# Kernel tuning notes

Measured on AMD Instinct MI355X. Metric: run time of the kernel, lower is better.

## Reference

```python
import jax, jax.numpy as jnp
import numpy as np

H = 16  # num_heads (inner_dim 1024 // default head_dim 64)
D = 64  # head_dim
EPS = 1e-5

def layernorm(x, w, b):
    mu = jnp.mean(x, axis=-1, keepdims=True)
    var = jnp.var(x, axis=-1, keepdims=True)
    return (x - mu) * jax.lax.rsqrt(var + EPS) * w + b

def attention(x, kv, wq, wk, wv, wo, bo):
    b, t, c = x.shape
    s = kv.shape[1]
    q = (x @ wq).reshape(b, t, H, D).transpose(0, 2, 1, 3)   # bhtd
    k = (kv @ wk).reshape(b, s, H, D).transpose(0, 2, 1, 3)  # bhsd
    v = (kv @ wv).reshape(b, s, H, D).transpose(0, 2, 1, 3)
    scores = jnp.einsum('bhqd,bhkd->bhqk', q, k) * (D ** -0.5)
    attn = jax.nn.softmax(scores, axis=-1)
    out = jnp.einsum('bhqk,bhkd->bhqd', attn, v)
    out = out.transpose(0, 2, 1, 3).reshape(b, t, c)
    return out @ wo + bo

def setup_inputs() -> dict:
    key = jax.random.key(0)
    ks = jax.random.split(key, 16)
    hs = 1024
    dff = 4 * hs  # 4096
    sc = lambda fan_in: 1.0 / np.sqrt(fan_in)
    inp = {
        'x': jax.random.normal(ks[0], (2, 2048, hs), jnp.float32),
        'encoder_hidden_states': jax.random.normal(ks[1], (2, 512, 64), jnp.float32),
        'ln1_w': jnp.ones((hs,), jnp.float32), 'ln1_b': jnp.zeros((hs,), jnp.float32),
        'a1_wq': jax.random.normal(ks[2], (hs, hs), jnp.float32) * sc(hs),
        'a1_wk': jax.random.normal(ks[3], (hs, hs), jnp.float32) * sc(hs),
        'a1_wv': jax.random.normal(ks[4], (hs, hs), jnp.float32) * sc(hs),
        'a1_wo': jax.random.normal(ks[5], (hs, hs), jnp.float32) * sc(hs),
        'a1_bo': jnp.zeros((hs,), jnp.float32),
        'ln2_w': jnp.ones((hs,), jnp.float32), 'ln2_b': jnp.zeros((hs,), jnp.float32),
        'a2_wq': jax.random.normal(ks[6], (hs, hs), jnp.float32) * sc(hs),
        'a2_wk': jax.random.normal(ks[7], (64, hs), jnp.float32) * sc(64),
        'a2_wv': jax.random.normal(ks[8], (64, hs), jnp.float32) * sc(64),
        'a2_wo': jax.random.normal(ks[9], (hs, hs), jnp.float32) * sc(hs),
        'a2_bo': jnp.zeros((hs,), jnp.float32),
        'ln3_w': jnp.ones((hs,), jnp.float32), 'ln3_b': jnp.zeros((hs,), jnp.float32),
        'ff_w1': jax.random.normal(ks[10], (hs, 2 * dff), jnp.float32) * sc(hs),
        'ff_b1': jnp.zeros((2 * dff,), jnp.float32),
        'ff_w2': jax.random.normal(ks[11], (dff, hs), jnp.float32) * sc(dff),
        'ff_b2': jnp.zeros((hs,), jnp.float32),
    }
    return inp

def reference(x, encoder_hidden_states, ln1_w, ln1_b, a1_wq, a1_wk, a1_wv, a1_wo, a1_bo,
              ln2_w, ln2_b, a2_wq, a2_wk, a2_wv, a2_wo, a2_bo,
              ln3_w, ln3_b, ff_w1, ff_b1, ff_w2, ff_b2):
    # self-attention sub-block
    h = layernorm(x, ln1_w, ln1_b)
    x = x + attention(h, h, a1_wq, a1_wk, a1_wv, a1_wo, a1_bo)
    # cross-attention sub-block (kv from encoder_hidden_states, dim 64)
    h = layernorm(x, ln2_w, ln2_b)
    x = x + attention(h, encoder_hidden_states, a2_wq, a2_wk, a2_wv, a2_wo, a2_bo)
    # GEGLU feed-forward sub-block
    h = layernorm(x, ln3_w, ln3_b)
    hp = h @ ff_w1 + ff_b1
    h1, h2 = jnp.split(hp, 2, axis=-1)
    h = (h1 * jax.nn.gelu(h2, approximate=False)) @ ff_w2 + ff_b2
    return x + h
```

## Files before the change

kernel.cpp:

```cpp
#include <hip/hip_runtime.h>
#include <hip/hip_bf16.h>
#include <stdint.h>

typedef unsigned short u16;
typedef __bf16 bf16x8 __attribute__((ext_vector_type(8)));
typedef float f32x4 __attribute__((ext_vector_type(4)));
typedef u16 u16x8 __attribute__((ext_vector_type(8)));
typedef u16 u16x4 __attribute__((ext_vector_type(4)));

__device__ __forceinline__ u16 f2bf(float f) {
  union { float f; uint32_t u; } v; v.f = f;
  uint32_t r = v.u + 0x7fffu + ((v.u >> 16) & 1u);
  return (u16)(r >> 16);
}
__device__ __forceinline__ float bf2f(u16 u) {
  union { uint32_t u; float f; } v; v.u = ((uint32_t)u) << 16;
  return v.f;
}
__device__ __forceinline__ uint32_t cvtpk(float a, float b) {
  uint32_t r;
  asm("v_cvt_pk_bf16_f32 %0, %1, %2" : "=v"(r) : "v"(a), "v"(b));
  return r;
}

__device__ __forceinline__ void gld16(const u16* g, u16* l) {
  __builtin_amdgcn_global_load_lds(
      (const __attribute__((address_space(1))) uint32_t*)g,
      (__attribute__((address_space(3))) uint32_t*)l, 16, 0, 0);
}

struct WB {
  const float* src[6];
  u16* dst[6];
  float scale[6];
};
__global__ void wconv_b(WB wb, int K, int N) {
  const int z = blockIdx.z;
  const float* __restrict__ W = wb.src[z];
  u16* __restrict__ Wt = wb.dst[z];
  const float scale = wb.scale[z];
  __shared__ float tile[32][33];
  const int n0 = blockIdx.x * 32, k0 = blockIdx.y * 32;
  const int tx = threadIdx.x, ty = threadIdx.y;
#pragma unroll
  for (int i = 0; i < 4; ++i)
    tile[ty + 8 * i][tx] = W[(size_t)(k0 + ty + 8 * i) * N + n0 + tx];
  __syncthreads();
#pragma unroll
  for (int i = 0; i < 4; ++i)
    Wt[(size_t)(n0 + ty + 8 * i) * K + k0 + tx] = f2bf(scale * tile[tx][ty + 8 * i]);
}

__global__ void wconv_t(const float* __restrict__ W, u16* __restrict__ Wt, int K, int N) {
  __shared__ float tile[32][33];
  const int n0 = blockIdx.x * 32, k0 = blockIdx.y * 32;
  const int tx = threadIdx.x, ty = threadIdx.y;
#pragma unroll
  for (int i = 0; i < 4; ++i)
    tile[ty + 8 * i][tx] = W[(size_t)(k0 + ty + 8 * i) * N + n0 + tx];
  __syncthreads();
#pragma unroll
  for (int i = 0; i < 4; ++i)
    Wt[(size_t)(n0 + ty + 8 * i) * K + k0 + tx] = f2bf(tile[tx][ty + 8 * i]);
}

__global__ void wconv_g(const float* __restrict__ W, u16* __restrict__ Wt) {
  __shared__ float tile[32][33];
  const int n0 = blockIdx.x * 32, k0 = blockIdx.y * 32;
  const int tx = threadIdx.x, ty = threadIdx.y;
#pragma unroll
  for (int i = 0; i < 4; ++i)
    tile[ty + 8 * i][tx] = W[(size_t)(k0 + ty + 8 * i) * 8192 + n0 + tx];
  __syncthreads();
#pragma unroll
  for (int i = 0; i < 4; ++i) {
    const int n = n0 + ty + 8 * i;
    const int half = n >> 12, c = n & 4095;
    const int blk = c >> 7, cc = c & 127;
    const int wcol = cc >> 5, rem = cc & 31;
    const int sub = rem >> 4, idx = rem & 15;
    const int p = blk * 256 + wcol * 64 + (sub * 2 + half) * 16 + idx;
    Wt[(size_t)p * 1024 + k0 + tx] = f2bf(tile[tx][ty + 8 * i]);
  }
}

__global__ void cvt_bf(const float* __restrict__ in, u16* __restrict__ out, int n) {
  int i = blockIdx.x * 256 + threadIdx.x;
  if (i < n) out[i] = f2bf(in[i]);
}

__global__ __launch_bounds__(256)
void vtrans(const u16* __restrict__ V, int ldv, int hoff, u16* __restrict__ Vt, int S) {
  __shared__ u16 tile[64][72];
  const int t0 = blockIdx.x, bh = blockIdx.y;
  const int b = bh >> 4, hc = (bh & 15) * 64 + hoff;
  const int tid = threadIdx.x;
  const int r = tid >> 2, dq = (tid & 3) * 16;
  const int pos = ((r >> 5) << 5) | (((r >> 2) & 3) << 3) | (((r >> 4) & 1) << 2) | (r & 3);
  const size_t grow = ((size_t)b * S + t0 * 64 + r) * ldv + hc + dq;
  u16x8 v1 = *(const u16x8*)&V[grow];
  u16x8 v2 = *(const u16x8*)&V[grow + 8];
#pragma unroll
  for (int j = 0; j < 8; ++j) {
    tile[dq + j][pos] = v1[j];
    tile[dq + 8 + j][pos] = v2[j];
  }
  __syncthreads();
  const int d = tid >> 2, c = (tid & 3) * 16;
  u16x8 o1, o2;
#pragma unroll
  for (int j = 0; j < 8; ++j) { o1[j] = tile[d][c + j]; o2[j] = tile[d][c + 8 + j]; }
  *(u16x8*)&Vt[((size_t)bh * 64 + d) * S + t0 * 64 + c] = o1;
  *(u16x8*)&Vt[((size_t)bh * 64 + d) * S + t0 * 64 + c + 8] = o2;
}

__global__ __launch_bounds__(256)
void ln_fwd(const float* __restrict__ X, const float* __restrict__ wt,
            const float* __restrict__ bs, u16* __restrict__ Y) {
  const int row = blockIdx.x, t = threadIdx.x;
  const float4 v = *(const float4*)&X[(size_t)row * 1024 + t * 4];
  float s = v.x + v.y + v.z + v.w;
  float s2 = v.x * v.x + v.y * v.y + v.z * v.z + v.w * v.w;
#pragma unroll
  for (int off = 32; off > 0; off >>= 1) {
    s += __shfl_xor(s, off);
    s2 += __shfl_xor(s2, off);
  }
  __shared__ float rs[4], rs2[4];
  const int w = t >> 6;
  if ((t & 63) == 0) { rs[w] = s; rs2[w] = s2; }
  __syncthreads();
  s = rs[0] + rs[1] + rs[2] + rs[3];
  s2 = rs2[0] + rs2[1] + rs2[2] + rs2[3];
  const float mu = s * (1.0f / 1024.0f);
  const float var = s2 * (1.0f / 1024.0f) - mu * mu;
  const float rstd = rsqrtf(var + 1e-5f);
  const float4 wv = *(const float4*)&wt[t * 4];
  const float4 bv = *(const float4*)&bs[t * 4];
  u16x4 o;
  o[0] = f2bf((v.x - mu) * rstd * wv.x + bv.x);
  o[1] = f2bf((v.y - mu) * rstd * wv.y + bv.y);
  o[2] = f2bf((v.z - mu) * rstd * wv.z + bv.z);
  o[3] = f2bf((v.w - mu) * rstd * wv.w + bv.w);
  *(u16x4*)&Y[(size_t)row * 1024 + t * 4] = o;
}

template<int TN>
__global__ __launch_bounds__(256, 4)
void gemm_bf16(const u16* __restrict__ A, int lda, const u16* __restrict__ Bt,
               int M, int N, int K, const float* __restrict__ bias,
               const float* __restrict__ resid, float oscale,
               float* __restrict__ outF, u16* __restrict__ outB) {
  constexpr int WNV = (TN == 128) ? 2 : 1;
  constexpr int WMV = 4 / WNV;
  constexpr int WM = 128 / WMV;
  constexpr int WN = TN / WNV;
  constexpr int MI = WM / 16, NI = WN / 16;
  __shared__ __align__(16) u16 Al[128 * 64];
  __shared__ __align__(16) u16 Bl[TN * 64];
  const int tid = threadIdx.x;
  const int w = tid >> 6, l = tid & 63, lo = l & 15, g = l >> 4;
  const int gx = gridDim.x, nwg = gx * gridDim.y;
  const int lin = blockIdx.y * gx + blockIdx.x;
  const int q = nwg >> 3, r = nwg & 7;
  const int xcd = lin & 7, pos = lin >> 3;
  const int sid = (xcd < r ? xcd * (q + 1) : r * (q + 1) + (xcd - r) * q) + pos;
  const int bm = (sid % gx) * 128, bn = (sid / gx) * TN;
  const int wm = (w / WNV) * WM, wn = (w % WNV) * WN;
  const int swz = (lo & 7) << 3;
  f32x4 acc[MI][NI] = {};

  for (int k0 = 0; k0 < K; k0 += 64) {
#pragma unroll
    for (int p = 0; p < 4; ++p) {
      int idx = p * 256 + tid;
      int row = idx >> 3, c = idx & 7;
      gld16(A + (size_t)(bm + row) * lda + k0 + ((c ^ (row & 7)) << 3), &Al[idx * 8]);
    }
#pragma unroll
    for (int p = 0; p < TN / 32; ++p) {
      int idx = p * 256 + tid;
      int row = idx >> 3, c = idx & 7;
      gld16(Bt + (size_t)(bn + row) * K + k0 + ((c ^ (row & 7)) << 3), &Bl[idx * 8]);
    }
    asm volatile("s_waitcnt vmcnt(0)" ::: "memory");
    __syncthreads();
#pragma unroll
    for (int ks = 0; ks < 2; ++ks) {
      bf16x8 af[MI], bf[NI];
#pragma unroll
      for (int i = 0; i < MI; ++i)
        af[i] = *(const bf16x8*)&Al[(wm + i * 16 + lo) * 64 + ((ks * 32 + g * 8) ^ swz)];
#pragma unroll
      for (int i = 0; i < NI; ++i)
        bf[i] = *(const bf16x8*)&Bl[(wn + i * 16 + lo) * 64 + ((ks * 32 + g * 8) ^ swz)];
#pragma unroll
      for (int mi = 0; mi < MI; ++mi)
#pragma unroll
        for (int ni = 0; ni < NI; ++ni)
          acc[mi][ni] = __builtin_amdgcn_mfma_f32_16x16x32_bf16(af[mi], bf[ni], acc[mi][ni], 0, 0, 0);
    }
    __syncthreads();
  }

#pragma unroll
  for (int mi = 0; mi < MI; ++mi) {
#pragma unroll
    for (int ni = 0; ni < NI; ++ni) {
      const int col = bn + wn + ni * 16 + lo;
      const float bb = bias ? bias[col] : 0.0f;
      const int row0 = bm + wm + mi * 16 + g * 4;
#pragma unroll
      for (int rr = 0; rr < 4; ++rr) {
        const size_t off = (size_t)(row0 + rr) * N + col;
        float v = acc[mi][ni][rr] * oscale + bb;
        if (resid) v += resid[off];
        if (outF) outF[off] = v;
        else outB[off] = f2bf(v);
      }
    }
  }
}

#define ST2(p0, p1, dst) { gld16(p0, (dst) + tid * 8); gld16(p1, (dst) + 4096 + tid * 8); (p0) += 64; (p1) += 64; }

template<int MODE>
__global__ __launch_bounds__(512, 2)
void gemm256(const u16* __restrict__ A, int lda, const u16* __restrict__ Bt,
             int M, int N, int K, const float* __restrict__ bias,
             const float* __restrict__ resid, float oscale,
             float* __restrict__ outF, u16* __restrict__ outB) {
  __shared__ __align__(16) u16 sm[65536];
  const int tid = threadIdx.x;
  const int w = tid >> 6, l = tid & 63, lo = l & 15, g = l >> 4;
  const int wrow = w >> 2, wcol = w & 3;
  const int gx = gridDim.x;
  const int nwg = gx * gridDim.y;
  const int lin = blockIdx.y * gx + blockIdx.x;
  const int q = nwg >> 3, r = nwg & 7;
  const int xcd = lin & 7, pos = lin >> 3;
  const int sid = (xcd < r ? xcd * (q + 1) : r * (q + 1) + (xcd - r) * q) + pos;
  const int bm = (sid % gx) * 256, bn = (sid / gx) * 256;

  const int NT = K >> 6;
  const int swz = (lo & 7) << 3;
  f32x4 acc[8][4] = {};

  const int sr8 = tid >> 3;
  const int sc8 = ((tid & 7) ^ (sr8 & 7)) << 3;
  const u16 *pA0 = A + (size_t)(bm + sr8) * lda + sc8;
  const u16 *pA1 = A + (size_t)(bm + 64 + sr8) * lda + sc8;
  const u16 *pA2 = A + (size_t)(bm + 128 + sr8) * lda + sc8;
  const u16 *pA3 = A + (size_t)(bm + 192 + sr8) * lda + sc8;
  const u16 *pB0 = Bt + (size_t)(bn + sr8) * K + sc8;
  const u16 *pB1 = Bt + (size_t)(bn + 64 + sr8) * K + sc8;
  const u16 *pB2 = Bt + (size_t)(bn + 128 + sr8) * K + sc8;
  const u16 *pB3 = Bt + (size_t)(bn + 192 + sr8) * K + sc8;

  ST2(pB0, pB1, sm + 16384);
  ST2(pB2, pB3, sm + 16384 + 8192);
  ST2(pA0, pA1, sm);
  ST2(pA2, pA3, sm + 8192);
  if (NT > 1) {
    ST2(pB0, pB1, sm + 32768 + 16384);
    ST2(pB2, pB3, sm + 32768 + 16384 + 8192);
    ST2(pA0, pA1, sm + 32768);
  }
  asm volatile("s_waitcnt vmcnt(6)" ::: "memory");
  __builtin_amdgcn_s_barrier();

  for (int t = 0; t < NT; ++t) {
    u16* Ab_ = sm + (t & 1) * 32768;
    u16* Bb_ = Ab_ + 16384;
    bf16x8 a0[4][2], a1[4][2], bfr[4][2];
#pragma unroll
    for (int mf = 0; mf < 4; ++mf) {
      const int rowi = wrow * 128 + mf * 16 + lo;
#pragma unroll
      for (int kk = 0; kk < 2; ++kk)
        a0[mf][kk] = *(const bf16x8*)&Ab_[rowi * 64 + ((kk * 32 + g * 8) ^ swz)];
    }
#pragma unroll
    for (int nf = 0; nf < 4; ++nf) {
      const int rowi = wcol * 64 + nf * 16 + lo;
#pragma unroll
      for (int kk = 0; kk < 2; ++kk)
        bfr[nf][kk] = *(const bf16x8*)&Bb_[rowi * 64 + ((kk * 32 + g * 8) ^ swz)];
    }
    if (t + 1 < NT)
      ST2(pA2, pA3, sm + ((t + 1) & 1) * 32768 + 8192);
    __builtin_amdgcn_s_barrier();
    __builtin_amdgcn_s_setprio(1);
#pragma unroll
    for (int mf = 0; mf < 4; ++mf)
#pragma unroll
      for (int nf = 0; nf < 2; ++nf)
#pragma unroll
        for (int kk = 0; kk < 2; ++kk)
          acc[mf][nf] = __builtin_amdgcn_mfma_f32_16x16x32_bf16(a0[mf][kk], bfr[nf][kk], acc[mf][nf], 0, 0, 0);
    __builtin_amdgcn_s_setprio(0);
    __builtin_amdgcn_s_barrier();
#pragma unroll
    for (int mf = 0; mf < 4; ++mf) {
      const int rowi = wrow * 128 + 64 + mf * 16 + lo;
#pragma unroll
      for (int kk = 0; kk < 2; ++kk)
        a1[mf][kk] = *(const bf16x8*)&Ab_[rowi * 64 + ((kk * 32 + g * 8) ^ swz)];
    }
    if (t + 2 < NT)
      ST2(pB0, pB1, sm + (t & 1) * 32768 + 16384);
    __builtin_amdgcn_s_barrier();
    __builtin_amdgcn_s_setprio(1);
#pragma unroll
    for (int mf = 0; mf < 4; ++mf)
#pragma unroll
      for (int nf = 2; nf < 4; ++nf)
#pragma unroll
        for (int kk = 0; kk < 2; ++kk)
          acc[mf][nf] = __builtin_amdgcn_mfma_f32_16x16x32_bf16(a0[mf][kk], bfr[nf][kk], acc[mf][nf], 0, 0, 0);
    __builtin_amdgcn_s_setprio(0);
    __builtin_amdgcn_s_barrier();
    if (t + 2 < NT)
      ST2(pB2, pB3, sm + (t & 1) * 32768 + 16384 + 8192);
    __builtin_amdgcn_s_barrier();
    __builtin_amdgcn_s_setprio(1);
#pragma unroll
    for (int mf = 0; mf < 4; ++mf)
#pragma unroll
      for (int nf = 0; nf < 2; ++nf)
#pragma unroll
        for (int kk = 0; kk < 2; ++kk)
          acc[4 + mf][nf] = __builtin_amdgcn_mfma_f32_16x16x32_bf16(a1[mf][kk], bfr[nf][kk], acc[4 + mf][nf], 0, 0, 0);
    __builtin_amdgcn_s_setprio(0);
    __builtin_amdgcn_s_barrier();
    if (t + 2 < NT)
      ST2(pA0, pA1, sm + (t & 1) * 32768);
    __builtin_amdgcn_s_barrier();
    __builtin_amdgcn_s_setprio(1);
#pragma unroll
    for (int mf = 0; mf < 4; ++mf)
#pragma unroll
      for (int nf = 2; nf < 4; ++nf)
#pragma unroll
        for (int kk = 0; kk < 2; ++kk)
          acc[4 + mf][nf] = __builtin_amdgcn_mfma_f32_16x16x32_bf16(a1[mf][kk], bfr[nf][kk], acc[4 + mf][nf], 0, 0, 0);
    __builtin_amdgcn_s_setprio(0);
    if (t + 2 < NT) asm volatile("s_waitcnt vmcnt(6)" ::: "memory");
    else            asm volatile("s_waitcnt vmcnt(0)" ::: "memory");
    __builtin_amdgcn_s_barrier();
  }

  if (MODE == 1) {
    const int obase = bn >> 1;
#pragma unroll
    for (int mi = 0; mi < 8; ++mi) {
#pragma unroll
      for (int sub = 0; sub < 2; ++sub) {
        const int col = obase + wcol * 32 + sub * 16 + lo;
        const float b1 = bias[col];
        const float b2 = bias[4096 + col];
#pragma unroll
        for (int rr = 0; rr < 4; ++rr) {
          const int rowi = wrow * 128 + mi * 16 + g * 4 + rr;
          const float h1 = acc[mi][sub * 2][rr] + b1;
          const float h2 = acc[mi][sub * 2 + 1][rr] + b2;
          const float ge = 0.5f * h2 * (1.0f + erff(h2 * 0.70710678118f));
          outB[(size_t)(bm + rowi) * 4096 + col] = f2bf(h1 * ge);
        }
      }
    }
    return;
  }

#pragma unroll
  for (int mi = 0; mi < 8; ++mi) {
#pragma unroll
    for (int ni = 0; ni < 4; ++ni) {
      const int col = bn + wcol * 64 + ni * 16 + lo;
      const float bb = bias ? bias[col] : 0.0f;
      const int row0 = bm + wrow * 128 + mi * 16 + g * 4;
#pragma unroll
      for (int rr = 0; rr < 4; ++rr) {
        const size_t off = (size_t)(row0 + rr) * N + col;
        float v = acc[mi][ni][rr] * oscale + bb;
        if (resid) v += resid[off];
        if (outF) outF[off] = v;
        else outB[off] = f2bf(v);
      }
    }
  }
}

#define ABODY(TT, KST, KRD, VST, VRD, SCur, SNxt)                                  \
  {                                                                                \
    if ((TT) + 2 < ntile) {                                                        \
      gld16(kp0, &KST[tid * 8]);                                                   \
      gld16(kp1, &KST[2048 + tid * 8]);                                            \
      kp0 += kadv; kp1 += kadv;                                                    \
    }                                                                              \
    if ((TT) + 1 < ntile) {                                                        \
      gld16(vp0, &VST[tid * 8]);                                                   \
      gld16(vp1, &VST[2048 + tid * 8]);                                            \
      vp0 += 64; vp1 += 64;                                                        \
    }                                                                              \
    if ((TT) + 2 < ntile)      asm volatile("s_waitcnt vmcnt(4)" ::: "memory");    \
    else if ((TT) + 1 < ntile) asm volatile("s_waitcnt vmcnt(2)" ::: "memory");    \
    else                       asm volatile("s_waitcnt vmcnt(0)" ::: "memory");    \
    __builtin_amdgcn_s_barrier();                                                  \
    if ((TT) + 1 < ntile) {                                                        \
      _Pragma("unroll")                                                            \
      for (int c = 0; c < 4; ++c) {                                                \
        f32x4 zz = {};                                                             \
        SNxt[c] = zz;                                                              \
        _Pragma("unroll")                                                          \
        for (int kk = 0; kk < 2; ++kk) {                                           \
          bf16x8 kf = *(const bf16x8*)&KRD[(c * 16 + lo) * 64 +                    \
                                           ((kk * 32 + g * 8) ^ ((lo & 7) << 3))]; \
          SNxt[c] = __builtin_amdgcn_mfma_f32_16x16x32_bf16(kf, qf[kk], SNxt[c], 0, 0, 0); \
        }                                                                          \
      }                                                                            \
    }                                                                              \
    float mx = fmaxf(fmaxf(fmaxf(SCur[0][0], SCur[0][1]), fmaxf(SCur[0][2], SCur[0][3])),  \
                     fmaxf(fmaxf(SCur[1][0], SCur[1][1]), fmaxf(SCur[1][2], SCur[1][3]))); \
    mx = fmaxf(mx, fmaxf(fmaxf(fmaxf(SCur[2][0], SCur[2][1]), fmaxf(SCur[2][2], SCur[2][3])),  \
                         fmaxf(fmaxf(SCur[3][0], SCur[3][1]), fmaxf(SCur[3][2], SCur[3][3])))); \
    mx = fmaxf(mx, __shfl_xor(mx, 16));                                            \
    mx = fmaxf(mx, __shfl_xor(mx, 32));                                            \
    if (!__all(mx <= m + 8.0f)) {                                                  \
      const float mn = fmaxf(m, mx);                                               \
      const float al = exp2f(m - mn);                                              \
      m = mn;                                                                      \
      f32x4 arv;                                                                   \
      _Pragma("unroll")                                                            \
      for (int rr = 0; rr < 4; ++rr) arv[rr] = __shfl(al, 20 * g + rr);            \
      _Pragma("unroll")                                                            \
      for (int dn = 0; dn < 4; ++dn) oa[dn] *= arv;                                \
      lrow *= arv;                                                                 \
    }                                                                              \
    _Pragma("unroll")                                                              \
    for (int c = 0; c < 4; ++c)                                                    \
      _Pragma("unroll")                                                            \
      for (int rr = 0; rr < 4; ++rr)                                               \
        SCur[c][rr] = exp2f(SCur[c][rr] - m);                                      \
    union { uint32_t u[4]; bf16x8 v; } af[2];                                      \
    _Pragma("unroll")                                                              \
    for (int ks = 0; ks < 2; ++ks) {                                               \
      af[ks].u[0] = cvtpk(SCur[2 * ks][0], SCur[2 * ks][1]);                       \
      af[ks].u[1] = cvtpk(SCur[2 * ks][2], SCur[2 * ks][3]);                       \
      af[ks].u[2] = cvtpk(SCur[2 * ks + 1][0], SCur[2 * ks + 1][1]);               \
      af[ks].u[3] = cvtpk(SCur[2 * ks + 1][2], SCur[2 * ks + 1][3]);               \
    }                                                                              \
    lrow = __builtin_amdgcn_mfma_f32_16x16x32_bf16(af[0].v, onesc.v, lrow, 0, 0, 0); \
    lrow = __builtin_amdgcn_mfma_f32_16x16x32_bf16(af[1].v, onesc.v, lrow, 0, 0, 0); \
    _Pragma("unroll")                                                              \
    for (int dn = 0; dn < 4; ++dn)                                                 \
      _Pragma("unroll")                                                            \
      for (int ks = 0; ks < 2; ++ks) {                                             \
        bf16x8 vf = *(const bf16x8*)&VRD[(dn * 16 + lo) * 64 +                     \
                                         ((ks * 32 + g * 8) ^ ((lo & 7) << 3))];   \
        oa[dn] = __builtin_amdgcn_mfma_f32_16x16x32_bf16(af[ks].v, vf, oa[dn], 0, 0, 0); \
      }                                                                            \
    asm volatile("s_waitcnt lgkmcnt(0)" ::: "memory");                             \
    __builtin_amdgcn_s_barrier();                                                  \
  }

__global__ __launch_bounds__(256, 4)
void attn_fwd(const u16* __restrict__ Q, int ldq, const u16* __restrict__ K, int ldk,
              const u16* __restrict__ Vt, u16* __restrict__ O, int T, int S) {
  __shared__ __align__(16) u16 Kl[2][4096];
  __shared__ __align__(16) u16 Vl[2][4096];
  const int tid = threadIdx.x, w = tid >> 6, l = tid & 63, lo = l & 15, g = l >> 4;
  const int nwg = gridDim.x * gridDim.y;
  const int n = blockIdx.y * gridDim.x + blockIdx.x;
  const int sid = (n & 7) * (nwg >> 3) + (n >> 3);
  const int qt = sid % gridDim.x, bh = sid / gridDim.x;
  const int b = bh >> 4, h = bh & 15, hc = h * 64;
  const int q0 = qt * 64 + w * 16;
  const size_t qrow = (size_t)b * T + q0;
  const size_t krow0 = (size_t)b * S;
  const size_t vrow0 = (size_t)bh * 64;

  bf16x8 qf[2];
#pragma unroll
  for (int kk = 0; kk < 2; ++kk)
    qf[kk] = *(const bf16x8*)&Q[(qrow + lo) * ldq + hc + kk * 32 + g * 8];

  union { u16 u[8]; bf16x8 v; } onesc;
#pragma unroll
  for (int j = 0; j < 8; ++j) onesc.u[j] = 0x3F80;

  f32x4 oa[4] = {};
  f32x4 lrow = {};
  float m = -1e30f;

  const int srow = tid >> 3;
  const int scol = (((tid & 7) ^ (srow & 7)) << 3);
  const int ntile = S >> 6;
  const size_t kadv = (size_t)64 * ldk;

  const u16* kp0 = K + (krow0 + 128 + srow) * ldk + hc + scol;
  const u16* kp1 = K + (krow0 + 160 + srow) * ldk + hc + scol;
  const u16* vp0 = Vt + (vrow0 + srow) * S + 64 + scol;
  const u16* vp1 = Vt + (vrow0 + 32 + srow) * S + 64 + scol;

#pragma unroll
  for (int c = 0; c < 2; ++c)
    gld16(K + (krow0 + c * 32 + srow) * ldk + hc + scol, &Kl[0][c * 2048 + tid * 8]);
#pragma unroll
  for (int c = 0; c < 2; ++c)
    gld16(K + (krow0 + 64 + c * 32 + srow) * ldk + hc + scol, &Kl[1][c * 2048 + tid * 8]);
#pragma unroll
  for (int c = 0; c < 2; ++c)
    gld16(Vt + (vrow0 + c * 32 + srow) * S + scol, &Vl[0][c * 2048 + tid * 8]);
  asm volatile("s_waitcnt vmcnt(0)" ::: "memory");
  __builtin_amdgcn_s_barrier();

  f32x4 sC[4] = {}, sN[4] = {};
#pragma unroll
  for (int c = 0; c < 4; ++c)
#pragma unroll
    for (int kk = 0; kk < 2; ++kk) {
      bf16x8 kf = *(const bf16x8*)&Kl[0][(c * 16 + lo) * 64 +
                                        ((kk * 32 + g * 8) ^ ((lo & 7) << 3))];
      sC[c] = __builtin_amdgcn_mfma_f32_16x16x32_bf16(kf, qf[kk], sC[c], 0, 0, 0);
    }
  asm volatile("s_waitcnt lgkmcnt(0)" ::: "memory");
  __builtin_amdgcn_s_barrier();

  for (int t0 = 0; t0 < ntile; t0 += 2) {
    ABODY(t0,     Kl[0], Kl[1], Vl[1], Vl[0], sC, sN)
    ABODY(t0 + 1, Kl[1], Kl[0], Vl[0], Vl[1], sN, sC)
  }

#pragma unroll
  for (int dn = 0; dn < 4; ++dn)
#pragma unroll
    for (int rr = 0; rr < 4; ++rr)
      O[(qrow + g * 4 + rr) * 1024 + hc + dn * 16 + lo] = f2bf(oa[dn][rr] / lrow[rr]);
}

extern "C" void kernel_launch(void* const* d_in, const int* in_sizes, int n_in,
                              void* d_out, int out_size, void* d_ws, size_t ws_size,
                              hipStream_t stream) {
  const float* x      = (const float*)d_in[0];
  const float* enc    = (const float*)d_in[1];
  const float* ln1_w  = (const float*)d_in[2];
  const float* ln1_b  = (const float*)d_in[3];
  const float* a1_wq  = (const float*)d_in[4];
  const float* a1_wk  = (const float*)d_in[5];
  const float* a1_wv  = (const float*)d_in[6];
  const float* a1_wo  = (const float*)d_in[7];
  const float* a1_bo  = (const float*)d_in[8];
  const float* ln2_w  = (const float*)d_in[9];
  const float* ln2_b  = (const float*)d_in[10];
  const float* a2_wq  = (const float*)d_in[11];
  const float* a2_wk  = (const float*)d_in[12];
  const float* a2_wv  = (const float*)d_in[13];
  const float* a2_wo  = (const float*)d_in[14];
  const float* a2_bo  = (const float*)d_in[15];
  const float* ln3_w  = (const float*)d_in[16];
  const float* ln3_b  = (const float*)d_in[17];
  const float* ff_w1  = (const float*)d_in[18];
  const float* ff_b1  = (const float*)d_in[19];
  const float* ff_w2  = (const float*)d_in[20];
  const float* ff_b2  = (const float*)d_in[21];

  char* ws = (char*)d_ws;
  const size_t MB = 1u << 20;
  u16* wqkv1t = (u16*)(ws + 0 * MB);
  u16* wo1t   = (u16*)(ws + 6 * MB);
  u16* wq2t   = (u16*)(ws + 8 * MB);
  u16* wo2t   = (u16*)(ws + 10 * MB);
  u16* wkv2t  = (u16*)(ws + 12 * MB);
  u16* encb   = (u16*)(ws + 12 * MB + 512 * 1024);
  u16* w1t    = (u16*)(ws + 13 * MB);
  u16* w2t    = (u16*)(ws + 29 * MB);
  float* x2   = (float*)(ws + 37 * MB);
  u16* Vt1    = (u16*)(ws + 37 * MB);
  u16* Vt2    = (u16*)(ws + 45 * MB);
  u16* KVb    = (u16*)(ws + 47 * MB);
  u16* hbuf   = (u16*)(ws + 53 * MB);
  u16* qkv    = (u16*)(ws + 61 * MB);
  u16* Qb     = (u16*)(ws + 61 * MB);
  u16* Ab     = (u16*)(ws + 85 * MB);
  float* x1   = (float*)(ws + 93 * MB);
  u16* gq     = (u16*)(ws + 61 * MB);

  const float SCL = 0.125f * 1.44269504f;
  const dim3 tb(32, 8);
  {
    WB wb;
    wb.src[0] = a1_wq; wb.dst[0] = wqkv1t;               wb.scale[0] = SCL;
    wb.src[1] = a1_wk; wb.dst[1] = wqkv1t + 1024 * 1024; wb.scale[1] = 1.0f;
    wb.src[2] = a1_wv; wb.dst[2] = wqkv1t + 2048 * 1024; wb.scale[2] = 1.0f;
    wb.src[3] = a1_wo; wb.dst[3] = wo1t;                 wb.scale[3] = 1.0f;
    wb.src[4] = a2_wq; wb.dst[4] = wq2t;                 wb.scale[4] = SCL;
    wb.src[5] = a2_wo; wb.dst[5] = wo2t;                 wb.scale[5] = 1.0f;
    wconv_b<<<dim3(32, 32, 6), tb, 0, stream>>>(wb, 1024, 1024);
    WB wb2;
    wb2.src[0] = a2_wk; wb2.dst[0] = wkv2t;             wb2.scale[0] = 1.0f;
    wb2.src[1] = a2_wv; wb2.dst[1] = wkv2t + 64 * 1024; wb2.scale[1] = 1.0f;
    wb2.src[2] = a2_wk; wb2.dst[2] = wkv2t;             wb2.scale[2] = 1.0f;
    wb2.src[3] = a2_wk; wb2.dst[3] = wkv2t;             wb2.scale[3] = 1.0f;
    wb2.src[4] = a2_wk; wb2.dst[4] = wkv2t;             wb2.scale[4] = 1.0f;
    wb2.src[5] = a2_wk; wb2.dst[5] = wkv2t;             wb2.scale[5] = 1.0f;
    wconv_b<<<dim3(32, 2, 2), tb, 0, stream>>>(wb2, 64, 1024);
  }
  wconv_g<<<dim3(256, 32), tb, 0, stream>>>(ff_w1, w1t);
  wconv_t<<<dim3(32, 128), tb, 0, stream>>>(ff_w2, w2t, 4096, 1024);
  cvt_bf<<<256, 256, 0, stream>>>(enc, encb, 2 * 512 * 64);

  ln_fwd<<<4096, 256, 0, stream>>>(x, ln1_w, ln1_b, hbuf);
  gemm256<0><<<dim3(16, 12), 512, 0, stream>>>(hbuf, 1024, wqkv1t, 4096, 3072, 1024, nullptr, nullptr, 1.0f, nullptr, qkv);
  vtrans<<<dim3(32, 32), 256, 0, stream>>>(qkv, 3072, 2048, Vt1, 2048);
  attn_fwd<<<dim3(32, 32), 256, 0, stream>>>(qkv, 3072, qkv + 1024, 3072, Vt1, Ab, 2048, 2048);
  gemm_bf16<64><<<dim3(32, 16), 256, 0, stream>>>(Ab, 1024, wo1t, 4096, 1024, 1024, a1_bo, x, 1.0f, x1, nullptr);

  ln_fwd<<<4096, 256, 0, stream>>>(x1, ln2_w, ln2_b, hbuf);
  gemm_bf16<64><<<dim3(32, 16), 256, 0, stream>>>(hbuf, 1024, wq2t, 4096, 1024, 1024, nullptr, nullptr, 1.0f, nullptr, Qb);
  gemm_bf16<64><<<dim3(8, 32), 256, 0, stream>>>(encb, 64, wkv2t, 1024, 2048, 64, nullptr, nullptr, 1.0f, nullptr, KVb);
  vtrans<<<dim3(8, 32), 256, 0, stream>>>(KVb + 1024, 2048, 0, Vt2, 512);
  attn_fwd<<<dim3(32, 32), 256, 0, stream>>>(Qb, 1024, KVb, 2048, Vt2, Ab, 2048, 512);
  gemm_bf16<64><<<dim3(32, 16), 256, 0, stream>>>(Ab, 1024, wo2t, 4096, 1024, 1024, a2_bo, x1, 1.0f, x2, nullptr);

  ln_fwd<<<4096, 256, 0, stream>>>(x2, ln3_w, ln3_b, hbuf);
  gemm256<1><<<dim3(16, 32), 512, 0, stream>>>(hbuf, 1024, w1t, 4096, 8192, 1024, ff_b1, nullptr, 1.0f, nullptr, gq);
  gemm_bf16<64><<<dim3(32, 16), 256, 0, stream>>>(gq, 4096, w2t, 4096, 1024, 4096, ff_b2, x2, 1.0f, (float*)d_out, nullptr);
}
```

Before: 409.7 us.

## Double-buffer LDS tiles in bf16 GEMM to overlap global loads with MFMA

```diff
diff --git a/kernel.cpp b/kernel.cpp
--- a/kernel.cpp
+++ b/kernel.cpp
@@ -145,8 +145,26 @@
   *(u16x4*)&Y[(size_t)row * 1024 + t * 4] = o;
 }
 
+#define GSTAGE(kt, bufi)                                                         \
+  {                                                                              \
+    _Pragma("unroll")                                                            \
+    for (int p = 0; p < 4; ++p) {                                                \
+      int idx = p * 256 + tid;                                                   \
+      int row = idx >> 3, c = idx & 7;                                           \
+      gld16(A + (size_t)(bm + row) * lda + (kt) * 64 + ((c ^ (row & 7)) << 3),   \
+            &Al[bufi][idx * 8]);                                                 \
+    }                                                                            \
+    _Pragma("unroll")                                                            \
+    for (int p = 0; p < TN / 32; ++p) {                                          \
+      int idx = p * 256 + tid;                                                   \
+      int row = idx >> 3, c = idx & 7;                                           \
+      gld16(Bt + (size_t)(bn + row) * K + (kt) * 64 + ((c ^ (row & 7)) << 3),    \
+            &Bl[bufi][idx * 8]);                                                 \
+    }                                                                            \
+  }
+
 template<int TN>
-__global__ __launch_bounds__(256, 4)
+__global__ __launch_bounds__(256, 3)
 void gemm_bf16(const u16* __restrict__ A, int lda, const u16* __restrict__ Bt,
                int M, int N, int K, const float* __restrict__ bias,
                const float* __restrict__ resid, float oscale,
@@ -156,8 +174,8 @@
   constexpr int WM = 128 / WMV;
   constexpr int WN = TN / WNV;
   constexpr int MI = WM / 16, NI = WN / 16;
-  __shared__ __align__(16) u16 Al[128 * 64];
-  __shared__ __align__(16) u16 Bl[TN * 64];
+  __shared__ __align__(16) u16 Al[2][128 * 64];
+  __shared__ __align__(16) u16 Bl[2][TN * 64];
   const int tid = threadIdx.x;
   const int w = tid >> 6, l = tid & 63, lo = l & 15, g = l >> 4;
   const int gx = gridDim.x, nwg = gx * gridDim.y;
@@ -168,38 +186,32 @@
   const int bm = (sid % gx) * 128, bn = (sid / gx) * TN;
   const int wm = (w / WNV) * WM, wn = (w % WNV) * WN;
   const int swz = (lo & 7) << 3;
+  const int NT = K >> 6;
   f32x4 acc[MI][NI] = {};
 
-  for (int k0 = 0; k0 < K; k0 += 64) {
-#pragma unroll
-    for (int p = 0; p < 4; ++p) {
-      int idx = p * 256 + tid;
-      int row = idx >> 3, c = idx & 7;
-      gld16(A + (size_t)(bm + row) * lda + k0 + ((c ^ (row & 7)) << 3), &Al[idx * 8]);
-    }
-#pragma unroll
-    for (int p = 0; p < TN / 32; ++p) {
-      int idx = p * 256 + tid;
-      int row = idx >> 3, c = idx & 7;
-      gld16(Bt + (size_t)(bn + row) * K + k0 + ((c ^ (row & 7)) << 3), &Bl[idx * 8]);
-    }
-    asm volatile("s_waitcnt vmcnt(0)" ::: "memory");
-    __syncthreads();
+  GSTAGE(0, 0);
+  asm volatile("s_waitcnt vmcnt(0)" ::: "memory");
+  __syncthreads();
+
+  for (int t = 0; t < NT; ++t) {
+    const int cur = t & 1;
+    if (t + 1 < NT) GSTAGE(t + 1, cur ^ 1);
 #pragma unroll
     for (int ks = 0; ks < 2; ++ks) {
       bf16x8 af[MI], bf[NI];
 #pragma unroll
       for (int i = 0; i < MI; ++i)
-        af[i] = *(const bf16x8*)&Al[(wm + i * 16 + lo) * 64 + ((ks * 32 + g * 8) ^ swz)];
+        af[i] = *(const bf16x8*)&Al[cur][(wm + i * 16 + lo) * 64 + ((ks * 32 + g * 8) ^ swz)];
 #pragma unroll
       for (int i = 0; i < NI; ++i)
-        bf[i] = *(const bf16x8*)&Bl[(wn + i * 16 + lo) * 64 + ((ks * 32 + g * 8) ^ swz)];
+        bf[i] = *(const bf16x8*)&Bl[cur][(wn + i * 16 + lo) * 64 + ((ks * 32 + g * 8) ^ swz)];
 #pragma unroll
       for (int mi = 0; mi < MI; ++mi)
 #pragma unroll
         for (int ni = 0; ni < NI; ++ni)
           acc[mi][ni] = __builtin_amdgcn_mfma_f32_16x16x32_bf16(af[mi], bf[ni], acc[mi][ni], 0, 0, 0);
     }
+    asm volatile("s_waitcnt vmcnt(0)" ::: "memory");
     __syncthreads();
   }
 
```

After: 397.9 us, median of 2. 2.9% less time.
